# Kernel optimization log

Measured on AMD Instinct MI355X. Metric: run time of the kernel, lower is better.

## Reference

```python
import jax, jax.numpy as jnp
import numpy as np

N = 100000; E = 200000; H = 64; P2 = 250000; P3 = 500000; G = 2048; NC = 10
NF = 18; EF = 18; Y = 0.25; EPS_BN = 1e-5


def setup_inputs() -> dict:
    key = jax.random.key(0)
    ks = jax.random.split(key, 20)
    def rn(i, shape, s=0.05):
        return jax.random.normal(ks[i], shape, jnp.float32) * s
    inp = {}
    inp["x"] = jax.random.normal(ks[0], (N, NF), jnp.float32)
    inp["edge_attr"] = jax.random.normal(ks[1], (E, EF), jnp.float32)
    inp["paths2"] = jax.random.randint(ks[2], (P2, 2), 0, N, jnp.int32)
    inp["ei2"] = jax.random.randint(ks[3], (P2, 1), 0, E, jnp.int32)
    inp["paths3"] = jax.random.randint(ks[4], (P3, 3), 0, N, jnp.int32)
    inp["ei3"] = jax.random.randint(ks[5], (P3, 2), 0, E, jnp.int32)
    inp["batch"] = jnp.sort(jax.random.randint(ks[6], (N,), 0, G, jnp.int32))
    inp["w_feat"] = rn(7, (NF, H)); inp["b_feat"] = jnp.zeros((H,), jnp.float32)
    inp["w_bond"] = rn(8, (EF, H)); inp["b_bond"] = jnp.zeros((H,), jnp.float32)
    inp["w_ih"] = rn(9, (4 * H, 2 * H)); inp["w_hh"] = rn(10, (4 * H, H))
    inp["b_ih"] = jnp.zeros((4 * H,), jnp.float32); inp["b_hh"] = jnp.zeros((4 * H,), jnp.float32)
    inp["bn_g"] = jnp.ones((2, H), jnp.float32); inp["bn_b"] = jnp.zeros((2, H), jnp.float32)
    inp["mlp_w1"] = rn(11, (2, H, H)); inp["mlp_b1"] = jnp.zeros((2, H), jnp.float32)
    inp["bn1_g"] = jnp.ones((2, H), jnp.float32); inp["bn1_b"] = jnp.zeros((2, H), jnp.float32)
    inp["mlp_w2"] = rn(12, (2, H, H)); inp["mlp_b2"] = jnp.zeros((2, H), jnp.float32)
    inp["bn2_g"] = jnp.ones((2, H), jnp.float32); inp["bn2_b"] = jnp.zeros((2, H), jnp.float32)
    inp["w_att"] = rn(13, (H,)); inp["b_att"] = jnp.zeros((1,), jnp.float32)
    inp["w_l1"] = rn(14, (H, H)); inp["b_l1"] = jnp.zeros((H,), jnp.float32)
    inp["w_l2"] = rn(15, (H, NC)); inp["b_l2"] = jnp.zeros((NC,), jnp.float32)
    return inp


def _batch_norm(x, g, b):
    # training-mode BN: biased batch statistics, eps=1e-5 (torch BatchNorm1d)
    m = x.mean(axis=0)
    v = x.var(axis=0)
    return (x - m) * jax.lax.rsqrt(v + EPS_BN) * g + b


def _lstm_final(x_seq, w_ih, w_hh, b_ih, b_hh):
    # x_seq: [P, L, 2H]; torch LSTM gate order i,f,g,o; return final hidden [P, H]
    P = x_seq.shape[0]
    Hd = w_hh.shape[1]
    def step(carry, xt):
        h, c = carry
        gates = xt @ w_ih.T + b_ih + h @ w_hh.T + b_hh
        i, f, g, o = jnp.split(gates, 4, axis=-1)
        c = jax.nn.sigmoid(f) * c + jax.nn.sigmoid(i) * jnp.tanh(g)
        h = jax.nn.sigmoid(o) * jnp.tanh(c)
        return (h, c), None
    h0 = jnp.zeros((P, Hd), x_seq.dtype)
    (h, _), _ = jax.lax.scan(step, (h0, h0), jnp.swapaxes(x_seq, 0, 1))
    return h


def _conv(i, x_in, ea_enc, paths, ei, w_ih, w_hh, b_ih, b_hh, bn_g, bn_b,
          mlp_w1, mlp_b1, bn1_g, bn1_b, mlp_w2, mlp_b2, bn2_g, bn2_b):
    P = paths.shape[0]
    ea = ea_enc[ei]                                        # [P, L-1, H]
    ea = jnp.concatenate([jnp.zeros((P, 1, H), ea.dtype), ea], axis=1)  # [P, L, H]
    x_cat = jnp.concatenate([x_in[paths], ea], axis=-1)    # [P, L, 2H]
    h = _lstm_final(x_cat, w_ih, w_hh, b_ih, b_hh)         # [P, H]
    h = jax.ops.segment_sum(h, paths[:, -1], num_segments=N)  # scatter_add to nodes
    h = _batch_norm(h, bn_g[i], bn_b[i])                   # residuals=False
    h = jax.nn.relu(_batch_norm(h @ mlp_w1[i] + mlp_b1[i], bn1_g[i], bn1_b[i]))
    h = jax.nn.relu(_batch_norm(h @ mlp_w2[i] + mlp_b2[i], bn2_g[i], bn2_b[i]))
    return h


def _attention(query, keys, w_att, b_att):
    scores = []
    for k in keys:
        s = jnp.sum(query * k, axis=0)                     # [H], sum over nodes
        s = (s - s.min()) / (s.max() - s.min() + 1e-6)
        scores.append(s @ w_att + b_att[0])                # scalar
    w = jax.nn.softmax(jnp.stack(scores))                  # [K]
    rep = sum(k * w[j] for j, k in enumerate(keys))
    return rep + query


def _forward(x, edge_attr, w_feat, b_feat, w_bond, b_bond, w_ih, w_hh, b_ih, b_hh,
             bn_g, bn_b, mlp_w1, mlp_b1, bn1_g, bn1_b, mlp_w2, mlp_b2, bn2_g, bn2_b,
             w_att, b_att, w_l1, b_l1, w_l2, b_l2, paths2, ei2, paths3, ei3, batch):
    W0 = x @ w_feat + b_feat                               # [N, H]
    ea_enc = edge_attr @ w_bond + b_bond                   # [E, H]
    common = (w_ih, w_hh, b_ih, b_hh, bn_g, bn_b, mlp_w1, mlp_b1, bn1_g, bn1_b,
              mlp_w2, mlp_b2, bn2_g, bn2_b)
    W1 = _conv(0, W0, ea_enc, paths2, ei2, *common)
    Win = (1.0 - Y) * W0 - Y * W1
    W2 = _conv(1, Win, ea_enc, paths3, ei3, *common)
    out = _attention(W0, [W1, W2], w_att, b_att)           # [N, H]
    out = jax.ops.segment_sum(out, batch, num_segments=G)  # global_add_pool -> [G, H]
    out = jax.nn.relu(out @ w_l1 + b_l1)
    return out @ w_l2 + b_l2                               # [G, NC]


def reference(x, edge_attr, paths2, ei2, paths3, ei3, batch, w_feat, b_feat,
              w_bond, b_bond, w_ih, w_hh, b_ih, b_hh, bn_g, bn_b, mlp_w1, mlp_b1,
              bn1_g, bn1_b, mlp_w2, mlp_b2, bn2_g, bn2_b, w_att, b_att,
              w_l1, b_l1, w_l2, b_l2):
    return _forward(x, edge_attr, w_feat, b_feat, w_bond, b_bond, w_ih, w_hh, b_ih, b_hh,
                    bn_g, bn_b, mlp_w1, mlp_b1, bn1_g, bn1_b, mlp_w2, mlp_b2, bn2_g, bn2_b,
                    w_att, b_att, w_l1, b_l1, w_l2, b_l2, paths2, ei2, paths3, ei3, batch)
```

## Files before the change

kernel.cpp:

```cpp
#include <hip/hip_runtime.h>
#include <math.h>

#define NNODES 100000
#define NEDGES 200000
#define HD 64
#define NP2 250000
#define NP3 500000
#define NG 2048
#define NCLS 10
#define NFEAT 18
#define EFEAT 18

typedef short short8v __attribute__((ext_vector_type(8)));
typedef float f32x4 __attribute__((ext_vector_type(4)));

__device__ __forceinline__ unsigned short bf16r(float a) {
    unsigned u = __builtin_bit_cast(unsigned, a);
    return (unsigned short)((u + 0x7FFFu + ((u >> 16) & 1u)) >> 16);
}

#define LOG2E 1.4426950408889634f

__global__ void prep_bias(const float* __restrict__ b_ih, const float* __restrict__ b_hh,
                          float* __restrict__ bsum) {
    int j = threadIdx.x;
    float s = ((j >> 6) == 2) ? 2.f * LOG2E : LOG2E;
    bsum[j] = (b_ih[j] + b_hh[j]) * s;
}

__global__ void prep_bp(const float* __restrict__ w_ih, const float* __restrict__ w_hh,
                        unsigned short* __restrict__ Bp) {
    int gid = blockIdx.x * 256 + threadIdx.x;
    if (gid >= 6 * 16 * 64 * 8) return;
    int kc = gid >> 13;
    int rem = gid & 8191;
    int nt = rem >> 9;
    int rem2 = rem & 511;
    int l = rem2 >> 3, j = rem2 & 7;
    int c = l & 15, q = l >> 4;
    int jh = nt >> 2, qg = nt & 3;
    int k = kc * 32 + q * 8 + j;
    int n = qg * 64 + 16 * jh + c;
    float f = (k < 128) ? w_ih[n * 128 + k] : w_hh[n * 64 + (k - 128)];
    float s = (qg == 2) ? 2.f * LOG2E : LOG2E;
    Bp[gid] = bf16r(f * s);
}

__global__ void encode_all(const float* __restrict__ X, const float* __restrict__ Wf,
                           const float* __restrict__ bf,
                           const float* __restrict__ Ea, const float* __restrict__ Wb,
                           const float* __restrict__ bb,
                           float* __restrict__ W0, unsigned short* __restrict__ W0b,
                           unsigned short* __restrict__ eab) {
    long gid = (long)blockIdx.x * 256 + threadIdx.x;
    if (gid >= (long)(NNODES + NEDGES) * 64) return;
    long r = gid >> 6;
    int col = (int)(gid & 63);
    if (r < NNODES) {
        float acc = bf[col];
        const float* xr = X + r * NFEAT;
        for (int k = 0; k < NFEAT; ++k) acc += xr[k] * Wf[k * 64 + col];
        W0[gid] = acc;
        W0b[gid] = bf16r(acc);
    } else {
        long r2 = r - NNODES;
        float acc = bb[col];
        const float* xr = Ea + r2 * EFEAT;
        for (int k = 0; k < EFEAT; ++k) acc += xr[k] * Wb[k * 64 + col];
        eab[r2 * 64 + col] = bf16r(acc);
    }
}

template <int L>
__global__ __launch_bounds__(256, 3)
void conv_mfma(const unsigned short* __restrict__ xb, const unsigned short* __restrict__ eab,
               const int* __restrict__ paths, const int* __restrict__ ei,
               const unsigned short* __restrict__ Bp, const float* __restrict__ bsum,
               float* __restrict__ hsum, int P) {
    __shared__ unsigned short Al[2][64 * 200];

    const int t = threadIdx.x;
    const int w = t >> 6, lane = t & 63;
    const int c = lane & 15, q = lane >> 4;
    const int pl = t >> 2, gq = t & 3;
    const long pg = (long)blockIdx.x * 64 + pl;
    const int pc = (pg < P) ? (int)pg : P - 1;

    const short8v* __restrict__ Bv = (const short8v*)Bp;
    const int bbase = (w * 4) * 64 + lane;

    float breg[4];
#pragma unroll
    for (int g2 = 0; g2 < 4; ++g2) breg[g2] = bsum[g2 * 64 + 16 * w + c];

    float creg[16];
#pragma unroll
    for (int i = 0; i < 16; ++i) creg[i] = 0.f;

    f32x4 acc[4][4];
    short8v bs0[4], bs1[4], bs2[4];
    uint4 nu0, nu1, ev0, ev1;

    {
        int node = paths[pc * L + 0];
        const uint4* s4 = (const uint4*)(xb + (size_t)node * HD);
        uint4 a0 = s4[2 * gq], a1 = s4[2 * gq + 1];
        *(uint4*)&Al[0][pl * 200 + gq * 16] = a0;
        *(uint4*)&Al[0][pl * 200 + gq * 16 + 8] = a1;
    }
    __syncthreads();

    int cur = 0;
    for (int step = 0; step < L; ++step) {
        const unsigned short* Ac = Al[cur];
        unsigned short* An = Al[cur ^ 1];

#pragma unroll
        for (int mt = 0; mt < 4; ++mt)
#pragma unroll
            for (int g2 = 0; g2 < 4; ++g2) {
                f32x4 v; v[0] = breg[g2]; v[1] = breg[g2]; v[2] = breg[g2]; v[3] = breg[g2];
                acc[mt][g2] = v;
            }

#define LOADB(BUF, KC)                                                         \
        { _Pragma("unroll")                                                    \
          for (int g2 = 0; g2 < 4; ++g2)                                       \
              BUF[g2] = Bv[(KC) * 1024 + g2 * 64 + bbase]; }

#define CHUNKS(BUF, KC)                                                        \
        { _Pragma("unroll")                                                    \
          for (int mt = 0; mt < 4; ++mt) {                                     \
              short8v af = *(const short8v*)&Ac[(mt * 16 + c) * 200 + (KC) * 32 + q * 8]; \
              _Pragma("unroll")                                                \
              for (int g2 = 0; g2 < 4; ++g2)                                   \
                  acc[mt][g2] = __builtin_amdgcn_mfma_f32_16x16x32_bf16(       \
                      af, BUF[g2], acc[mt][g2], 0, 0, 0);                      \
          } }

        if (step == 0) {
            LOADB(bs0, 0)
            LOADB(bs1, 1)
            {
                int node = paths[pc * L + 1];
                const uint4* s4 = (const uint4*)(xb + (size_t)node * HD);
                nu0 = s4[2 * gq]; nu1 = s4[2 * gq + 1];
                int e = ei[pc * (L - 1) + 0];
                const uint4* e4 = (const uint4*)(eab + (size_t)e * HD);
                ev0 = e4[2 * gq]; ev1 = e4[2 * gq + 1];
            }
            CHUNKS(bs0, 0)
            CHUNKS(bs1, 1)
        } else {
            LOADB(bs0, 0)
            LOADB(bs1, 1)
            LOADB(bs2, 2)
            CHUNKS(bs0, 0) LOADB(bs0, 3)
            CHUNKS(bs1, 1) LOADB(bs1, 4)
            CHUNKS(bs2, 2) LOADB(bs2, 5)
            if (step + 1 < L) {
                int node = paths[pc * L + step + 1];
                const uint4* s4 = (const uint4*)(xb + (size_t)node * HD);
                nu0 = s4[2 * gq]; nu1 = s4[2 * gq + 1];
                int e = ei[pc * (L - 1) + step];
                const uint4* e4 = (const uint4*)(eab + (size_t)e * HD);
                ev0 = e4[2 * gq]; ev1 = e4[2 * gq + 1];
            }
            CHUNKS(bs0, 3)
            CHUNKS(bs1, 4)
            CHUNKS(bs2, 5)
        }
#undef LOADB
#undef CHUNKS

#pragma unroll
        for (int mt = 0; mt < 4; ++mt) {
#pragma unroll
            for (int r = 0; r < 4; ++r) {
                float gi = acc[mt][0][r], gf = acc[mt][1][r];
                float gg = acc[mt][2][r], go = acc[mt][3][r];
                float ea = __builtin_amdgcn_exp2f(-gf);
                float eb = __builtin_amdgcn_exp2f(-gi);
                float ed = __builtin_amdgcn_exp2f(-gg);
                float eo = __builtin_amdgcn_exp2f(-go);
                float pa = 1.f + ea, pb = 1.f + eb, pd = 1.f + ed;
                float cn = (creg[mt * 4 + r] * pb * pd + (1.f - ed) * pa) *
                           __builtin_amdgcn_rcpf(pa * pb * pd);
                creg[mt * 4 + r] = cn;
                float et = __builtin_amdgcn_exp2f(-2.8853900817779268f * cn);
                float hn = (1.f - et) *
                           __builtin_amdgcn_rcpf((1.f + eo) * (1.f + et));
                if (step < L - 1) {
                    An[(mt * 16 + q * 4 + r) * 200 + 128 + 16 * w + c] = bf16r(hn);
                } else {
                    long pr = (long)blockIdx.x * 64 + mt * 16 + q * 4 + r;
                    if (pr < P) {
                        int node = paths[pr * L + (L - 1)];
                        atomicAdd(hsum + (size_t)node * HD + 16 * w + c, hn);
                    }
                }
            }
        }

        if (step + 1 < L) {
            *(uint4*)&An[pl * 200 + gq * 16] = nu0;
            *(uint4*)&An[pl * 200 + gq * 16 + 8] = nu1;
            *(uint4*)&An[pl * 200 + 64 + gq * 16] = ev0;
            *(uint4*)&An[pl * 200 + 64 + gq * 16 + 8] = ev1;
            __syncthreads();
        }
        cur ^= 1;
    }
}

__global__ void col_stats(const float* __restrict__ X, int nrows, float* __restrict__ out) {
    int col = threadIdx.x & 63, rg = threadIdx.x >> 6;
    float s = 0.f, q = 0.f;
    long stride = (long)gridDim.x * 4;
    for (long r = (long)blockIdx.x * 4 + rg; r < nrows; r += stride) {
        float v = X[r * 64 + col];
        s += v;
        q += v * v;
    }
    __shared__ float red[2][256];
    red[0][threadIdx.x] = s;
    red[1][threadIdx.x] = q;
    __syncthreads();
    if (threadIdx.x < 64) {
        int c = threadIdx.x;
        float ss = red[0][c] + red[0][c + 64] + red[0][c + 128] + red[0][c + 192];
        float qq = red[1][c] + red[1][c + 64] + red[1][c + 128] + red[1][c + 192];
        atomicAdd(out + c, ss);
        atomicAdd(out + 64 + c, qq);
    }
}

__device__ __forceinline__ void bn_affine(const float* stats, const float* g,
                                          const float* b, int col, int nrows,
                                          float& a, float& c) {
    float inv = 1.0f / (float)nrows;
    float mean = stats[col] * inv;
    float var = stats[64 + col] * inv - mean * mean;
    a = g[col] * rsqrtf(var + 1e-5f);
    c = b[col] - mean * a;
}

template <bool INRELU, bool STATS>
__global__ __launch_bounds__(256)
void gemm64(const float* __restrict__ X, const float* __restrict__ stats_in,
            const float* __restrict__ bn_gm, const float* __restrict__ bn_bt,
            const float* __restrict__ W, const float* __restrict__ bias,
            float* __restrict__ Y, float* stats, int nrows) {
    __shared__ float Xs[64 * 64];
    __shared__ float red[2][256];
    const int t = threadIdx.x;
    const int col = t & 63, rg = t >> 6;
    const long r0 = (long)blockIdx.x * 64;

    float a = 1.f, c = 0.f;
    if (stats_in) bn_affine(stats_in, bn_gm, bn_bt, col, nrows, a, c);

    for (int i = 0; i < 16; ++i) {
        int rl = rg * 16 + i;
        long r = r0 + rl;
        float v = (r < nrows) ? X[r * 64 + col] : 0.f;
        v = v * a + c;
        if (INRELU) v = fmaxf(v, 0.f);
        Xs[rl * 64 + col] = v;
    }
    __syncthreads();

    float wreg[64];
#pragma unroll
    for (int k = 0; k < 64; ++k) wreg[k] = W[k * 64 + col];
    float bs = bias[col];
    float ssum = 0.f, ssq = 0.f;

    for (int i = 0; i < 16; ++i) {
        int rl = rg * 16 + i;
        long r = r0 + rl;
        const float4* xs4 = (const float4*)(Xs + rl * 64);
        float acc = bs;
#pragma unroll
        for (int k4 = 0; k4 < 16; ++k4) {
            float4 xv = xs4[k4];
            acc += xv.x * wreg[4 * k4] + xv.y * wreg[4 * k4 + 1] +
                   xv.z * wreg[4 * k4 + 2] + xv.w * wreg[4 * k4 + 3];
        }
        if (r < nrows) {
            Y[r * 64 + col] = acc;
            ssum += acc;
            ssq += acc * acc;
        }
    }
    if (STATS) {
        red[0][t] = ssum;
        red[1][t] = ssq;
        __syncthreads();
        if (t < 64) {
            float s = red[0][t] + red[0][t + 64] + red[0][t + 128] + red[0][t + 192];
            float qq = red[1][t] + red[1][t + 64] + red[1][t + 128] + red[1][t + 192];
            atomicAdd(stats + t, s);
            atomicAdd(stats + 64 + t, qq);
        }
    }
}

__global__ void bn_apply1(float* __restrict__ W1, const float* __restrict__ stats,
                          const float* __restrict__ g, const float* __restrict__ b,
                          const float* __restrict__ W0, unsigned short* __restrict__ Winb,
                          long n) {
    long gid = (long)blockIdx.x * 256 + threadIdx.x;
    if (gid >= n * 64) return;
    int col = (int)(gid & 63);
    float a, c;
    bn_affine(stats, g, b, col, (int)n, a, c);
    float v = fmaxf(W1[gid] * a + c, 0.f);
    W1[gid] = v;
    Winb[gid] = bf16r(0.75f * W0[gid] - 0.25f * v);
}

__global__ void bn_apply_att(float* __restrict__ W2, const float* __restrict__ stats,
                             const float* __restrict__ g, const float* __restrict__ b,
                             const float* __restrict__ W0, const float* __restrict__ W1,
                             float* __restrict__ atts, int n) {
    int col = threadIdx.x & 63, rg = threadIdx.x >> 6;
    float a, c;
    bn_affine(stats, g, b, col, n, a, c);
    float s1 = 0.f, s2 = 0.f;
    long stride = (long)gridDim.x * 4;
    for (long r = (long)blockIdx.x * 4 + rg; r < n; r += stride) {
        long gid = r * 64 + col;
        float v = fmaxf(W2[gid] * a + c, 0.f);
        W2[gid] = v;
        float q0 = W0[gid];
        s1 += q0 * W1[gid];
        s2 += q0 * v;
    }
    __shared__ float red[2][256];
    red[0][threadIdx.x] = s1;
    red[1][threadIdx.x] = s2;
    __syncthreads();
    if (threadIdx.x < 64) {
        int cc = threadIdx.x;
        float a1 = red[0][cc] + red[0][cc + 64] + red[0][cc + 128] + red[0][cc + 192];
        float a2 = red[1][cc] + red[1][cc + 64] + red[1][cc + 128] + red[1][cc + 192];
        atomicAdd(atts + cc, a1);
        atomicAdd(atts + 64 + cc, a2);
    }
}

__global__ void att_softmax(const float* __restrict__ atts, const float* __restrict__ w_att,
                            const float* __restrict__ b_att, float* __restrict__ watt) {
    int h = threadIdx.x;
    float z[2];
    for (int k = 0; k < 2; ++k) {
        float s = atts[64 * k + h];
        float mn = s, mx = s;
        for (int off = 32; off > 0; off >>= 1) {
            mn = fminf(mn, __shfl_down(mn, off));
            mx = fmaxf(mx, __shfl_down(mx, off));
        }
        mn = __shfl(mn, 0);
        mx = __shfl(mx, 0);
        float sn = (s - mn) / (mx - mn + 1e-6f);
        float d = sn * w_att[h];
        for (int off = 32; off > 0; off >>= 1) d += __shfl_down(d, off);
        z[k] = __shfl(d, 0) + b_att[0];
    }
    if (h == 0) {
        float m = fmaxf(z[0], z[1]);
        float e0 = expf(z[0] - m), e1 = expf(z[1] - m);
        float inv = 1.0f / (e0 + e1);
        watt[0] = e0 * inv;
        watt[1] = e1 * inv;
    }
}

#define PROWS 128
__global__ void pool_rep(const float* __restrict__ W0, const float* __restrict__ W1,
                         const float* __restrict__ W2, const float* __restrict__ watt,
                         const int* __restrict__ batch, float* __restrict__ pooled, int n) {
    int col = threadIdx.x & 63, rg = threadIdx.x >> 6;
    long r0 = (long)blockIdx.x * PROWS;
    float w1 = watt[0], w2 = watt[1];
    float acc = 0.f;
    int curg = -1;
    for (int i = rg; i < PROWS; i += 4) {
        long r = r0 + i;
        if (r >= n) break;
        int g = batch[r];
        long gid = r * 64 + col;
        float rep = W0[gid] + w1 * W1[gid] + w2 * W2[gid];
        if (g != curg) {
            if (curg >= 0) atomicAdd(pooled + (size_t)curg * 64 + col, acc);
            curg = g;
            acc = 0.f;
        }
        acc += rep;
    }
    if (curg >= 0) atomicAdd(pooled + (size_t)curg * 64 + col, acc);
}

__global__ __launch_bounds__(256)
void head_kernel(const float* __restrict__ pooled, const float* __restrict__ w_l1,
                 const float* __restrict__ b_l1, const float* __restrict__ w_l2,
                 const float* __restrict__ b_l2, float* __restrict__ out) {
    __shared__ float Xs[64 * 64];
    __shared__ float Ys[64 * 65];
    const int t = threadIdx.x;
    const int col = t & 63, rg = t >> 6;
    const int r0 = blockIdx.x * 64;

    for (int i = 0; i < 16; ++i) {
        int rl = rg * 16 + i;
        Xs[rl * 64 + col] = fmaxf(pooled[(size_t)(r0 + rl) * 64 + col], 0.f);
    }
    __syncthreads();

    float wreg[64];
#pragma unroll
    for (int k = 0; k < 64; ++k) wreg[k] = w_l1[k * 64 + col];
    float bs = b_l1[col];

    for (int i = 0; i < 16; ++i) {
        int rl = rg * 16 + i;
        const float4* xs4 = (const float4*)(Xs + rl * 64);
        float acc = bs;
#pragma unroll
        for (int k4 = 0; k4 < 16; ++k4) {
            float4 xv = xs4[k4];
            acc += xv.x * wreg[4 * k4] + xv.y * wreg[4 * k4 + 1] +
                   xv.z * wreg[4 * k4 + 2] + xv.w * wreg[4 * k4 + 3];
        }
        Ys[rl * 65 + col] = fmaxf(acc, 0.f);
    }
    __syncthreads();

    for (int idx = t; idx < 64 * NCLS; idx += 256) {
        int row = idx / NCLS, j = idx - row * NCLS;
        float acc = b_l2[j];
#pragma unroll
        for (int k = 0; k < 64; ++k) acc += Ys[row * 65 + k] * w_l2[k * NCLS + j];
        out[(size_t)(r0 + row) * NCLS + j] = acc;
    }
}

extern "C" void kernel_launch(void* const* d_in, const int* in_sizes, int n_in,
                              void* d_out, int out_size, void* d_ws, size_t ws_size,
                              hipStream_t stream) {
    const float* x         = (const float*)d_in[0];
    const float* edge_attr = (const float*)d_in[1];
    const int*   paths2    = (const int*)d_in[2];
    const int*   ei2       = (const int*)d_in[3];
    const int*   paths3    = (const int*)d_in[4];
    const int*   ei3       = (const int*)d_in[5];
    const int*   batch     = (const int*)d_in[6];
    const float* w_feat    = (const float*)d_in[7];
    const float* b_feat    = (const float*)d_in[8];
    const float* w_bond    = (const float*)d_in[9];
    const float* b_bond    = (const float*)d_in[10];
    const float* w_ih      = (const float*)d_in[11];
    const float* w_hh      = (const float*)d_in[12];
    const float* b_ih      = (const float*)d_in[13];
    const float* b_hh      = (const float*)d_in[14];
    const float* bn_g      = (const float*)d_in[15];
    const float* bn_b      = (const float*)d_in[16];
    const float* mlp_w1    = (const float*)d_in[17];
    const float* mlp_b1    = (const float*)d_in[18];
    const float* bn1_g     = (const float*)d_in[19];
    const float* bn1_b     = (const float*)d_in[20];
    const float* mlp_w2    = (const float*)d_in[21];
    const float* mlp_b2    = (const float*)d_in[22];
    const float* bn2_g     = (const float*)d_in[23];
    const float* bn2_b     = (const float*)d_in[24];
    const float* w_att     = (const float*)d_in[25];
    const float* b_att     = (const float*)d_in[26];
    const float* w_l1      = (const float*)d_in[27];
    const float* b_l1      = (const float*)d_in[28];
    const float* w_l2      = (const float*)d_in[29];
    const float* b_l2      = (const float*)d_in[30];

    const size_t N64 = (size_t)NNODES * 64;
    float* ws = (float*)d_ws;
    float* W0     = ws;
    float* W1     = W0 + N64;
    float* W2     = W1 + N64;
    float* Wtmp   = W2 + N64;
    float* hsum1  = Wtmp + N64;
    float* hsum2  = hsum1 + N64;
    unsigned short* W0b  = (unsigned short*)(hsum2 + N64);
    unsigned short* Winb = W0b + N64;
    unsigned short* eab  = Winb + N64;
    unsigned short* Bp   = eab + (size_t)NEDGES * 64;
    float* bsum   = (float*)(Bp + 6 * 16 * 64 * 8);
    float* st     = bsum + 256;
    float* atts   = st + 6 * 128;
    float* watt   = atts + 128;
    float* pooled = watt + 64;

    hipMemsetAsync(st, 0, (6 * 128 + 128 + 64) * sizeof(float), stream);
    hipMemsetAsync(pooled, 0, (size_t)NG * 64 * sizeof(float), stream);
    hipMemsetAsync(hsum1, 0, 2 * N64 * sizeof(float), stream);

    prep_bias<<<1, 256, 0, stream>>>(b_ih, b_hh, bsum);
    prep_bp<<<192, 256, 0, stream>>>(w_ih, w_hh, Bp);
    encode_all<<<(int)(((size_t)(NNODES + NEDGES) * 64 + 255) / 256), 256, 0, stream>>>(
        x, w_feat, b_feat, edge_attr, w_bond, b_bond, W0, W0b, eab);

    conv_mfma<2><<<(NP2 + 63) / 64, 256, 0, stream>>>(W0b, eab, paths2, ei2, Bp, bsum, hsum1, NP2);

    col_stats<<<1024, 256, 0, stream>>>(hsum1, NNODES, st + 0);
    gemm64<false, true><<<(NNODES + 63) / 64, 256, 0, stream>>>(hsum1, st + 0, bn_g + 0, bn_b + 0, mlp_w1, mlp_b1, Wtmp, st + 128, NNODES);
    gemm64<true, true><<<(NNODES + 63) / 64, 256, 0, stream>>>(Wtmp, st + 128, bn1_g + 0, bn1_b + 0, mlp_w2, mlp_b2, W1, st + 256, NNODES);
    bn_apply1<<<(NNODES * 64 + 255) / 256, 256, 0, stream>>>(W1, st + 256, bn2_g + 0, bn2_b + 0, W0, Winb, NNODES);

    conv_mfma<3><<<(NP3 + 63) / 64, 256, 0, stream>>>(Winb, eab, paths3, ei3, Bp, bsum, hsum2, NP3);

    col_stats<<<1024, 256, 0, stream>>>(hsum2, NNODES, st + 384);
    gemm64<false, true><<<(NNODES + 63) / 64, 256, 0, stream>>>(hsum2, st + 384, bn_g + 64, bn_b + 64, mlp_w1 + 4096, mlp_b1 + 64, Wtmp, st + 512, NNODES);
    gemm64<true, true><<<(NNODES + 63) / 64, 256, 0, stream>>>(Wtmp, st + 512, bn1_g + 64, bn1_b + 64, mlp_w2 + 4096, mlp_b2 + 64, W2, st + 640, NNODES);
    bn_apply_att<<<1024, 256, 0, stream>>>(W2, st + 640, bn2_g + 64, bn2_b + 64, W0, W1, atts, NNODES);

    att_softmax<<<1, 64, 0, stream>>>(atts, w_att, b_att, watt);
    pool_rep<<<(NNODES + PROWS - 1) / PROWS, 256, 0, stream>>>(W0, W1, W2, watt, batch, pooled, NNODES);
    head_kernel<<<NG / 64, 256, 0, stream>>>(pooled, w_l1, b_l1, w_l2, b_l2, (float*)d_out);
}
```

Before: 775.1 us.

## Merge prep kernels with memsets, fold softmax into pooling, restructure LSTM B loads

The two weight-prep kernels and two memsets become a single prep_all launch that also zeroes the stats and pooled buffers. The attention softmax is recomputed redundantly in every pool_rep block, removing a separate single-block launch. In conv_mfma, the first K-chunk of the gate weights stays in registers across steps and seeds the MFMA accumulators with the bias directly, using two rotating B buffers instead of three. The next-node and next-edge gathers move after all MFMA chunks, which may reduce overlap of those loads with compute.

```diff
diff --git a/kernel.cpp b/kernel.cpp
--- a/kernel.cpp
+++ b/kernel.cpp
@@ -21,29 +21,33 @@
 
 #define LOG2E 1.4426950408889634f
 
-__global__ void prep_bias(const float* __restrict__ b_ih, const float* __restrict__ b_hh,
-                          float* __restrict__ bsum) {
-    int j = threadIdx.x;
-    float s = ((j >> 6) == 2) ? 2.f * LOG2E : LOG2E;
-    bsum[j] = (b_ih[j] + b_hh[j]) * s;
-}
-
-__global__ void prep_bp(const float* __restrict__ w_ih, const float* __restrict__ w_hh,
-                        unsigned short* __restrict__ Bp) {
-    int gid = blockIdx.x * 256 + threadIdx.x;
-    if (gid >= 6 * 16 * 64 * 8) return;
-    int kc = gid >> 13;
-    int rem = gid & 8191;
-    int nt = rem >> 9;
-    int rem2 = rem & 511;
-    int l = rem2 >> 3, j = rem2 & 7;
-    int c = l & 15, q = l >> 4;
-    int jh = nt >> 2, qg = nt & 3;
-    int k = kc * 32 + q * 8 + j;
-    int n = qg * 64 + 16 * jh + c;
-    float f = (k < 128) ? w_ih[n * 128 + k] : w_hh[n * 64 + (k - 128)];
-    float s = (qg == 2) ? 2.f * LOG2E : LOG2E;
-    Bp[gid] = bf16r(f * s);
+__global__ void prep_all(const float* __restrict__ w_ih, const float* __restrict__ w_hh,
+                         const float* __restrict__ b_ih, const float* __restrict__ b_hh,
+                         unsigned short* __restrict__ Bp, float* __restrict__ bsum,
+                         float* __restrict__ zsmall, float* __restrict__ pooled) {
+    int b = blockIdx.x;
+    int t = threadIdx.x;
+    if (b < 192) {
+        int gid = b * 256 + t;
+        int kc = gid >> 13;
+        int rem = gid & 8191;
+        int nt = rem >> 9;
+        int rem2 = rem & 511;
+        int l = rem2 >> 3, j = rem2 & 7;
+        int c = l & 15, q = l >> 4;
+        int jh = nt >> 2, qg = nt & 3;
+        int k = kc * 32 + q * 8 + j;
+        int n = qg * 64 + 16 * jh + c;
+        float f = (k < 128) ? w_ih[n * 128 + k] : w_hh[n * 64 + (k - 128)];
+        float s = (qg == 2) ? 2.f * LOG2E : LOG2E;
+        Bp[gid] = bf16r(f * s);
+    } else if (b == 192) {
+        float s = ((t >> 6) == 2) ? 2.f * LOG2E : LOG2E;
+        bsum[t] = (b_ih[t] + b_hh[t]) * s;
+        for (int i = t; i < 960; i += 256) zsmall[i] = 0.f;
+    } else {
+        pooled[(b - 193) * 256 + t] = 0.f;
+    }
 }
 
 __global__ void encode_all(const float* __restrict__ X, const float* __restrict__ Wf,
@@ -87,46 +91,49 @@
     const int pc = (pg < P) ? (int)pg : P - 1;
 
     const short8v* __restrict__ Bv = (const short8v*)Bp;
-    const int bbase = (w * 4) * 64 + lane;
-
-    float breg[4];
-#pragma unroll
-    for (int g2 = 0; g2 < 4; ++g2) breg[g2] = bsum[g2 * 64 + 16 * w + c];
+    const int bbase = w * 256 + lane;
+
+    short8v Bk0[4];
+#pragma unroll
+    for (int g2 = 0; g2 < 4; ++g2) Bk0[g2] = Bv[g2 * 64 + bbase];
+    f32x4 bfr[4];
+#pragma unroll
+    for (int g2 = 0; g2 < 4; ++g2) {
+        float b = bsum[g2 * 64 + 16 * w + c];
+        f32x4 v; v[0] = b; v[1] = b; v[2] = b; v[3] = b;
+        bfr[g2] = v;
+    }
 
     float creg[16];
 #pragma unroll
     for (int i = 0; i < 16; ++i) creg[i] = 0.f;
 
     f32x4 acc[4][4];
-    short8v bs0[4], bs1[4], bs2[4];
+    short8v s0[4], s1[4];
     uint4 nu0, nu1, ev0, ev1;
 
     {
         int node = paths[pc * L + 0];
         const uint4* s4 = (const uint4*)(xb + (size_t)node * HD);
-        uint4 a0 = s4[2 * gq], a1 = s4[2 * gq + 1];
-        *(uint4*)&Al[0][pl * 200 + gq * 16] = a0;
-        *(uint4*)&Al[0][pl * 200 + gq * 16 + 8] = a1;
-    }
-    __syncthreads();
-
-    int cur = 0;
-    for (int step = 0; step < L; ++step) {
-        const unsigned short* Ac = Al[cur];
-        unsigned short* An = Al[cur ^ 1];
-
-#pragma unroll
-        for (int mt = 0; mt < 4; ++mt)
-#pragma unroll
-            for (int g2 = 0; g2 < 4; ++g2) {
-                f32x4 v; v[0] = breg[g2]; v[1] = breg[g2]; v[2] = breg[g2]; v[3] = breg[g2];
-                acc[mt][g2] = v;
-            }
+        *(uint4*)&Al[0][pl * 200 + gq * 16] = s4[2 * gq];
+        *(uint4*)&Al[0][pl * 200 + gq * 16 + 8] = s4[2 * gq + 1];
+    }
+    __syncthreads();
 
 #define LOADB(BUF, KC)                                                         \
         { _Pragma("unroll")                                                    \
           for (int g2 = 0; g2 < 4; ++g2)                                       \
               BUF[g2] = Bv[(KC) * 1024 + g2 * 64 + bbase]; }
+
+#define CHUNKB(BUF, KC)                                                        \
+        { _Pragma("unroll")                                                    \
+          for (int mt = 0; mt < 4; ++mt) {                                     \
+              short8v af = *(const short8v*)&Ac[(mt * 16 + c) * 200 + (KC) * 32 + q * 8]; \
+              _Pragma("unroll")                                                \
+              for (int g2 = 0; g2 < 4; ++g2)                                   \
+                  acc[mt][g2] = __builtin_amdgcn_mfma_f32_16x16x32_bf16(       \
+                      af, BUF[g2], bfr[g2], 0, 0, 0);                          \
+          } }
 
 #define CHUNKS(BUF, KC)                                                        \
         { _Pragma("unroll")                                                    \
@@ -138,40 +145,33 @@
                       af, BUF[g2], acc[mt][g2], 0, 0, 0);                      \
           } }
 
+    int cur = 0;
+    for (int step = 0; step < L; ++step) {
+        const unsigned short* Ac = Al[cur];
+        unsigned short* An = Al[cur ^ 1];
+
         if (step == 0) {
-            LOADB(bs0, 0)
-            LOADB(bs1, 1)
-            {
-                int node = paths[pc * L + 1];
-                const uint4* s4 = (const uint4*)(xb + (size_t)node * HD);
-                nu0 = s4[2 * gq]; nu1 = s4[2 * gq + 1];
-                int e = ei[pc * (L - 1) + 0];
-                const uint4* e4 = (const uint4*)(eab + (size_t)e * HD);
-                ev0 = e4[2 * gq]; ev1 = e4[2 * gq + 1];
-            }
-            CHUNKS(bs0, 0)
-            CHUNKS(bs1, 1)
+            LOADB(s0, 1)
+            CHUNKB(Bk0, 0)
+            CHUNKS(s0, 1)
         } else {
-            LOADB(bs0, 0)
-            LOADB(bs1, 1)
-            LOADB(bs2, 2)
-            CHUNKS(bs0, 0) LOADB(bs0, 3)
-            CHUNKS(bs1, 1) LOADB(bs1, 4)
-            CHUNKS(bs2, 2) LOADB(bs2, 5)
-            if (step + 1 < L) {
-                int node = paths[pc * L + step + 1];
-                const uint4* s4 = (const uint4*)(xb + (size_t)node * HD);
-                nu0 = s4[2 * gq]; nu1 = s4[2 * gq + 1];
-                int e = ei[pc * (L - 1) + step];
-                const uint4* e4 = (const uint4*)(eab + (size_t)e * HD);
-                ev0 = e4[2 * gq]; ev1 = e4[2 * gq + 1];
-            }
-            CHUNKS(bs0, 3)
-            CHUNKS(bs1, 4)
-            CHUNKS(bs2, 5)
-        }
-#undef LOADB
-#undef CHUNKS
+            LOADB(s0, 1) LOADB(s1, 2)
+            CHUNKB(Bk0, 0)
+            CHUNKS(s0, 1) LOADB(s0, 3)
+            CHUNKS(s1, 2) LOADB(s1, 4)
+            CHUNKS(s0, 3) LOADB(s0, 5)
+            CHUNKS(s1, 4)
+            CHUNKS(s0, 5)
+        }
+
+        if (step + 1 < L) {
+            int node = paths[pc * L + step + 1];
+            const uint4* s4 = (const uint4*)(xb + (size_t)node * HD);
+            nu0 = s4[2 * gq]; nu1 = s4[2 * gq + 1];
+            int e = ei[pc * (L - 1) + step];
+            const uint4* e4 = (const uint4*)(eab + (size_t)e * HD);
+            ev0 = e4[2 * gq]; ev1 = e4[2 * gq + 1];
+        }
 
 #pragma unroll
         for (int mt = 0; mt < 4; ++mt) {
@@ -211,6 +211,9 @@
         }
         cur ^= 1;
     }
+#undef LOADB
+#undef CHUNKB
+#undef CHUNKS
 }
 
 __global__ void col_stats(const float* __restrict__ X, int nrows, float* __restrict__ out) {
@@ -350,40 +353,41 @@
     }
 }
 
-__global__ void att_softmax(const float* __restrict__ atts, const float* __restrict__ w_att,
-                            const float* __restrict__ b_att, float* __restrict__ watt) {
-    int h = threadIdx.x;
-    float z[2];
-    for (int k = 0; k < 2; ++k) {
-        float s = atts[64 * k + h];
-        float mn = s, mx = s;
-        for (int off = 32; off > 0; off >>= 1) {
-            mn = fminf(mn, __shfl_down(mn, off));
-            mx = fmaxf(mx, __shfl_down(mx, off));
-        }
-        mn = __shfl(mn, 0);
-        mx = __shfl(mx, 0);
-        float sn = (s - mn) / (mx - mn + 1e-6f);
-        float d = sn * w_att[h];
-        for (int off = 32; off > 0; off >>= 1) d += __shfl_down(d, off);
-        z[k] = __shfl(d, 0) + b_att[0];
-    }
-    if (h == 0) {
-        float m = fmaxf(z[0], z[1]);
-        float e0 = expf(z[0] - m), e1 = expf(z[1] - m);
-        float inv = 1.0f / (e0 + e1);
-        watt[0] = e0 * inv;
-        watt[1] = e1 * inv;
-    }
-}
-
 #define PROWS 128
 __global__ void pool_rep(const float* __restrict__ W0, const float* __restrict__ W1,
-                         const float* __restrict__ W2, const float* __restrict__ watt,
+                         const float* __restrict__ W2, const float* __restrict__ atts,
+                         const float* __restrict__ w_att, const float* __restrict__ b_att,
                          const int* __restrict__ batch, float* __restrict__ pooled, int n) {
+    __shared__ float wsh[2];
+    if (threadIdx.x < 64) {
+        int h = threadIdx.x;
+        float z[2];
+        for (int k = 0; k < 2; ++k) {
+            float s = atts[64 * k + h];
+            float mn = s, mx = s;
+            for (int off = 32; off > 0; off >>= 1) {
+                mn = fminf(mn, __shfl_down(mn, off));
+                mx = fmaxf(mx, __shfl_down(mx, off));
+            }
+            mn = __shfl(mn, 0);
+            mx = __shfl(mx, 0);
+            float sn = (s - mn) / (mx - mn + 1e-6f);
+            float d = sn * w_att[h];
+            for (int off = 32; off > 0; off >>= 1) d += __shfl_down(d, off);
+            z[k] = __shfl(d, 0) + b_att[0];
+        }
+        if (h == 0) {
+            float m = fmaxf(z[0], z[1]);
+            float e0 = expf(z[0] - m), e1 = expf(z[1] - m);
+            float inv = 1.0f / (e0 + e1);
+            wsh[0] = e0 * inv;
+            wsh[1] = e1 * inv;
+        }
+    }
+    __syncthreads();
     int col = threadIdx.x & 63, rg = threadIdx.x >> 6;
     long r0 = (long)blockIdx.x * PROWS;
-    float w1 = watt[0], w2 = watt[1];
+    float w1 = wsh[0], w2 = wsh[1];
     float acc = 0.f;
     int curg = -1;
     for (int i = rg; i < PROWS; i += 4) {
@@ -499,12 +503,9 @@
     float* watt   = atts + 128;
     float* pooled = watt + 64;
 
-    hipMemsetAsync(st, 0, (6 * 128 + 128 + 64) * sizeof(float), stream);
-    hipMemsetAsync(pooled, 0, (size_t)NG * 64 * sizeof(float), stream);
     hipMemsetAsync(hsum1, 0, 2 * N64 * sizeof(float), stream);
 
-    prep_bias<<<1, 256, 0, stream>>>(b_ih, b_hh, bsum);
-    prep_bp<<<192, 256, 0, stream>>>(w_ih, w_hh, Bp);
+    prep_all<<<193 + 512, 256, 0, stream>>>(w_ih, w_hh, b_ih, b_hh, Bp, bsum, st, pooled);
     encode_all<<<(int)(((size_t)(NNODES + NEDGES) * 64 + 255) / 256), 256, 0, stream>>>(
         x, w_feat, b_feat, edge_attr, w_bond, b_bond, W0, W0b, eab);
 
@@ -522,7 +523,6 @@
     gemm64<true, true><<<(NNODES + 63) / 64, 256, 0, stream>>>(Wtmp, st + 512, bn1_g + 64, bn1_b + 64, mlp_w2 + 4096, mlp_b2 + 64, W2, st + 640, NNODES);
     bn_apply_att<<<1024, 256, 0, stream>>>(W2, st + 640, bn2_g + 64, bn2_b + 64, W0, W1, atts, NNODES);
 
-    att_softmax<<<1, 64, 0, stream>>>(atts, w_att, b_att, watt);
-    pool_rep<<<(NNODES + PROWS - 1) / PROWS, 256, 0, stream>>>(W0, W1, W2, watt, batch, pooled, NNODES);
+    pool_rep<<<(NNODES + PROWS - 1) / PROWS, 256, 0, stream>>>(W0, W1, W2, atts, w_att, b_att, batch, pooled, NNODES);
     head_kernel<<<NG / 64, 256, 0, stream>>>(pooled, w_l1, b_l1, w_l2, b_l2, (float*)d_out);
 }
```

Result: no change. 775.7 us (+0.1%).
